# Kernel optimization log

Hardware: AMD Instinct MI355X
Metric: run time of the kernel (lower is better)

The kernel has to match this reference:

```python
import jax, jax.numpy as jnp
import numpy as np

D_MODEL = 1024
D_FF = 4096
BATCH = 4
SEQ = 2048
DECAY = 0.9
THRESH = 0.5


def setup_inputs() -> dict:
    key = jax.random.key(0)
    k1, k2, k3, k4 = jax.random.split(key, 4)
    spikes = jax.random.normal(k1, (BATCH, SEQ, D_MODEL), dtype=jnp.float32)
    # xavier-ish init scales matching gains 0.5/0.5/0.3 in the torch module
    s1 = 0.5 * np.sqrt(2.0 / (D_MODEL + D_FF))
    s2 = 0.5 * np.sqrt(2.0 / (D_MODEL + D_FF))
    sr = 0.3 * np.sqrt(2.0 / (D_MODEL + D_FF))
    W1 = jax.random.normal(k2, (D_FF, D_MODEL), dtype=jnp.float32) * s1
    W2 = jax.random.normal(k3, (D_MODEL, D_FF), dtype=jnp.float32) * s2
    Wr = jax.random.normal(k4, (D_FF, D_MODEL), dtype=jnp.float32) * sr
    return {"spikes": spikes, "W1": W1, "W2": W2, "Wr": Wr}


def reference(spikes, W1, W2, Wr):
    # spikes: [B, T, D]; W1, Wr: [F, D]; W2: [D, F]
    B, T, D = spikes.shape
    F = W1.shape[0]
    d = jnp.float32(DECAY)
    one_minus_d = jnp.float32(1.0 - DECAY)
    # Hoist time-independent projections out of the recurrence (same math as
    # the per-timestep nn.Linear calls in the torch loop).
    r_all = jax.nn.sigmoid(jnp.einsum('btd,fd->btf', spikes, Wr))  # [B,T,F]
    h_all = jnp.einsum('btd,fd->btf', spikes, W1)                   # [B,T,F]

    def step(carry, xs):
        act, rec = carry              # [B,F] each, init zeros (fresh buffers)
        r_t, h_t = xs                 # [B,F]
        rec = d * rec + one_minus_d * r_t                 # mixed receptance
        mixed = d * act + one_minus_d * h_t               # temporal state mix
        spike = (mixed > THRESH).astype(h_t.dtype)        # eval-mode spikes
        gated = spike * r_t
        # torch detaches current_activation each step
        return (jax.lax.stop_gradient(mixed), rec), gated

    init = (jnp.zeros((B, F), spikes.dtype), jnp.zeros((B, F), spikes.dtype))
    _, gated = jax.lax.scan(step,
                            init,
                            (jnp.swapaxes(r_all, 0, 1), jnp.swapaxes(h_all, 0, 1)))
    # gated: [T, B, F] -> output [B, T, D]
    out = jnp.einsum('tbf,df->btd', gated, W2)
    return out
```

## Files before the change

### kernel.cpp

```cpp
#include <hip/hip_runtime.h>
#include <math.h>

#define B_    4
#define T_    2048
#define D_    1024
#define F_    4096
#define R_    (B_*T_)
#define SEG_  64
#define L_    (T_/SEG_)
#define DECAYF 0.9f
#define OMDF   0.1f
#define FLAG_THRESH 0.45f

typedef __attribute__((ext_vector_type(4)))  int   i32x4;
typedef __attribute__((ext_vector_type(8)))  int   i32x8;
typedef __attribute__((ext_vector_type(16))) float f32x16;

__device__ __forceinline__ int pk_fp8x4(float x, float y, float z, float w) {
    int p = 0;
    p = __builtin_amdgcn_cvt_pk_fp8_f32(x, y, p, false);
    p = __builtin_amdgcn_cvt_pk_fp8_f32(z, w, p, true);
    return p;
}

__device__ __forceinline__ size_t pk_off(int row, int d) {
    return ((size_t)((row >> 5) * 16 + (d >> 6)) * 2048)
         + ((d >> 4) & 1) * 1024
         + ((row & 31) + ((d >> 5) & 1) * 32) * 16
         + (d & 15);
}

#define KA_W1_BLOCKS  4096
#define KA_SEG_BLOCKS 256
#define KA_FLAG_BLOCKS 32

__global__ __launch_bounds__(256)
void kA_prologue(const float* __restrict__ spikes,
                 const float* __restrict__ W1,
                 unsigned char* __restrict__ w_f8,
                 float* __restrict__ seg_sum,
                 unsigned int* __restrict__ flags) {
    const int bid = blockIdx.x;
    const int tid = threadIdx.x;
    if (bid < KA_W1_BLOCKS) {
        int i = bid * 256 + tid;
        float4 v = ((const float4*)W1)[i];
        int f  = i >> 8;
        int d0 = (i & 255) * 4;
        *(int*)(w_f8 + pk_off(f, d0)) = pk_fp8x4(8.f*v.x, 8.f*v.y, 8.f*v.z, 8.f*v.w);
    } else if (bid < KA_W1_BLOCKS + KA_SEG_BLOCKS) {
        int t = (bid - KA_W1_BLOCKS) * 256 + tid;
        int dg = t & (D_ / 4 - 1);
        int s = (t >> 8) & (SEG_ - 1);
        int b = t >> 14;
        const float4* sp4 = (const float4*)spikes;
        const int base = (b * T_ + s * L_) * (D_ / 4) + dg;
        float4 e = {0.f, 0.f, 0.f, 0.f};
#pragma unroll 8
        for (int k = 0; k < L_; ++k) {
            float4 x = sp4[base + k * (D_ / 4)];
            e.x = DECAYF * e.x + OMDF * x.x;
            e.y = DECAYF * e.y + OMDF * x.y;
            e.z = DECAYF * e.z + OMDF * x.z;
            e.w = DECAYF * e.w + OMDF * x.w;
        }
        ((float4*)seg_sum)[(b * SEG_ + s) * (D_ / 4) + dg] = e;
    } else {
        int i = (bid - KA_W1_BLOCKS - KA_SEG_BLOCKS) * 256 + tid;
        if (i < R_) flags[i] = 0u;
    }
}

__global__ __launch_bounds__(256)
void kB_seg_scan(const float* __restrict__ seg_sum,
                 float* __restrict__ start_state) {
    int g = blockIdx.x * 256 + threadIdx.x;
    int s = g & 63;
    int c = g >> 6;
    int d = c & (D_ - 1);
    int b = c >> 10;
    int idx = (b * SEG_ + s) * D_ + d;
    float v = seg_sum[idx];
    float wp = 0.0343368382f;
#pragma unroll
    for (int off = 1; off < SEG_; off <<= 1) {
        float u = __shfl_up(v, off, 64);
        if (s >= off) v += wp * u;
        wp *= wp;
    }
    float pv = __shfl_up(v, 1, 64);
    start_state[idx] = (s == 0) ? 0.f : pv;
}

__global__ __launch_bounds__(256)
void kC_ema_fp8(const float* __restrict__ spikes,
                const float* __restrict__ start_state,
                unsigned char* __restrict__ a_f8) {
    int t = blockIdx.x * 256 + threadIdx.x;
    int dg = t & (D_ / 4 - 1);
    int s = (t >> 8) & (SEG_ - 1);
    int b = t >> 14;
    const float4* sp4 = (const float4*)spikes;
    const int base = (b * T_ + s * L_) * (D_ / 4) + dg;
    const int d0 = dg * 4;
    unsigned char* dst = a_f8 + pk_off(b * T_ + s * L_, d0);
    float4 e = ((const float4*)start_state)[(b * SEG_ + s) * (D_ / 4) + dg];
#pragma unroll 8
    for (int k = 0; k < L_; ++k) {
        float4 x = sp4[base + k * (D_ / 4)];
        e.x = DECAYF * e.x + OMDF * x.x;
        e.y = DECAYF * e.y + OMDF * x.y;
        e.z = DECAYF * e.z + OMDF * x.z;
        e.w = DECAYF * e.w + OMDF * x.w;
        *(int*)(dst + k * 16) = pk_fp8x4(8.f*e.x, 8.f*e.y, 8.f*e.z, 8.f*e.w);
    }
}

__global__ __launch_bounds__(256)
void k2_mfma_flags(const unsigned char* __restrict__ Ap,
                   const unsigned char* __restrict__ Bp,
                   unsigned int* __restrict__ flags) {
    const int tid = threadIdx.x;
    const int w = tid >> 6;
    const int lane = tid & 63;
    const int orig = blockIdx.x;
    const int xcd  = orig & 7;
    const int id   = orig >> 3;
    const int mt   = (xcd >> 1) * 16 + (id >> 4);
    const int nt   = (xcd & 1) * 16 + (id & 15);
    const int m0 = mt * 128;
    const int n0 = nt * 128;
    const int wm = w >> 1, wn = w & 1;
    const int kg = lane >> 5;

    const unsigned char* pa0 = Ap + ((size_t)((m0 >> 5) + wm * 2 + 0) * 16) * 2048 + lane * 16;
    const unsigned char* pa1 = Ap + ((size_t)((m0 >> 5) + wm * 2 + 1) * 16) * 2048 + lane * 16;
    const unsigned char* pb0 = Bp + ((size_t)((n0 >> 5) + wn * 2 + 0) * 16) * 2048 + lane * 16;
    const unsigned char* pb1 = Bp + ((size_t)((n0 >> 5) + wn * 2 + 1) * 16) * 2048 + lane * 16;

    f32x16 acc[2][2] = {};

#define LDFRAG(p, C)                                                        \
    ({ i32x4 lo_ = *(const i32x4*)((p) + (size_t)(C) * 2048);               \
       i32x4 hi_ = *(const i32x4*)((p) + (size_t)(C) * 2048 + 1024);        \
       (i32x8){lo_.x, lo_.y, lo_.z, lo_.w, hi_.x, hi_.y, hi_.z, hi_.w}; })

#define MFMA4(AF0, AF1, BF0, BF1)                                           \
    {                                                                       \
        acc[0][0] = __builtin_amdgcn_mfma_scale_f32_32x32x64_f8f6f4(        \
            AF0, BF0, acc[0][0], 0, 0, 0, 124, 0, 124);                     \
        acc[0][1] = __builtin_amdgcn_mfma_scale_f32_32x32x64_f8f6f4(        \
            AF0, BF1, acc[0][1], 0, 0, 0, 124, 0, 124);                     \
        acc[1][0] = __builtin_amdgcn_mfma_scale_f32_32x32x64_f8f6f4(        \
            AF1, BF0, acc[1][0], 0, 0, 0, 124, 0, 124);                     \
        acc[1][1] = __builtin_amdgcn_mfma_scale_f32_32x32x64_f8f6f4(        \
            AF1, BF1, acc[1][1], 0, 0, 0, 124, 0, 124);                     \
    }

#pragma unroll
    for (int C = 0; C < 16; ++C) {
        __syncthreads();
        __builtin_amdgcn_sched_barrier(0);
        i32x8 A0 = LDFRAG(pa0, C), A1 = LDFRAG(pa1, C);
        i32x8 B0 = LDFRAG(pb0, C), B1 = LDFRAG(pb1, C);
        MFMA4(A0, A1, B0, B1);
    }
#undef LDFRAG
#undef MFMA4

#pragma unroll
    for (int i = 0; i < 2; ++i) {
#pragma unroll
        for (int reg = 0; reg < 16; ++reg) {
            float mx = fmaxf(acc[i][0][reg], acc[i][1][reg]);
            if (mx > FLAG_THRESH) {
                const int rr = (reg & 3) + 8 * (reg >> 2) + 4 * kg;
                atomicOr(&flags[m0 + wm * 64 + i * 32 + rr], 1u);
            }
        }
    }
}

__global__ __launch_bounds__(256)
void k4_output(const float* __restrict__ spikes,
               const float* __restrict__ start_state,
               const float* __restrict__ W1,
               const float* __restrict__ Wr,
               const float* __restrict__ W2,
               const unsigned int* __restrict__ flags,
               float* __restrict__ out) {
    const int row = blockIdx.x;
    const int tid = threadIdx.x;
    float4 o = {0.f, 0.f, 0.f, 0.f};

    if (flags[row] == 0u) {
        *(float4*)&out[(size_t)row * D_ + tid * 4] = o;
        return;
    }

    __shared__ float se[D_];
    __shared__ float sp[D_];
    __shared__ float red[256];
    __shared__ int nspk;
    __shared__ int spk_list[256];

    const int b = row / T_;
    const int t = row % T_;
    const int seg = t / L_;
    const int off = t % L_;
    const int segbase = (b * T_ + seg * L_) * D_;

    for (int i = tid; i < D_; i += 256) {
        float e = start_state[(b * SEG_ + seg) * D_ + i];
        for (int j = 0; j <= off; ++j)
            e = DECAYF * e + OMDF * spikes[segbase + j * D_ + i];
        se[i] = e;
        sp[i] = spikes[(size_t)row * D_ + i];
    }
    if (tid == 0) nspk = 0;
    __syncthreads();

    for (int f0 = 0; f0 < F_; f0 += 256) {
        int f = f0 + tid;
        float mix = 0.f;
        for (int k = 0; k < D_; ++k) mix += se[k] * W1[(size_t)f * D_ + k];
        if (mix > 0.5f) {
            int idx = atomicAdd(&nspk, 1);
            spk_list[idx] = f;
        }
        __syncthreads();
        int n = nspk;
        for (int i = 0; i < n; ++i) {
            int fs = spk_list[i];
            float part = 0.f;
#pragma unroll
            for (int k = 0; k < 4; ++k)
                part += sp[tid * 4 + k] * Wr[(size_t)fs * D_ + tid * 4 + k];
            red[tid] = part;
            __syncthreads();
            for (int sft = 128; sft > 0; sft >>= 1) {
                if (tid < sft) red[tid] += red[tid + sft];
                __syncthreads();
            }
            float r = 1.f / (1.f + expf(-red[0]));
            __syncthreads();
            o.x += r * W2[(size_t)(tid * 4 + 0) * F_ + fs];
            o.y += r * W2[(size_t)(tid * 4 + 1) * F_ + fs];
            o.z += r * W2[(size_t)(tid * 4 + 2) * F_ + fs];
            o.w += r * W2[(size_t)(tid * 4 + 3) * F_ + fs];
        }
        __syncthreads();
        if (tid == 0) nspk = 0;
        __syncthreads();
    }
    *(float4*)&out[(size_t)row * D_ + tid * 4] = o;
}

extern "C" void kernel_launch(void* const* d_in, const int* in_sizes, int n_in,
                              void* d_out, int out_size, void* d_ws, size_t ws_size,
                              hipStream_t stream) {
    const float* spikes = (const float*)d_in[0];
    const float* W1     = (const float*)d_in[1];
    const float* W2     = (const float*)d_in[2];
    const float* Wr     = (const float*)d_in[3];
    float* out = (float*)d_out;

    char* ws = (char*)d_ws;
    float* seg_sum      = (float*)ws;
    float* start_state  = seg_sum + (size_t)B_ * SEG_ * D_;
    unsigned int* flags = (unsigned int*)(start_state + (size_t)B_ * SEG_ * D_);
    unsigned char* a_f8 = (unsigned char*)(flags + R_);
    unsigned char* w_f8 = a_f8 + (size_t)R_ * D_;

    kA_prologue<<<KA_W1_BLOCKS + KA_SEG_BLOCKS + KA_FLAG_BLOCKS, 256, 0, stream>>>(
        spikes, W1, w_f8, seg_sum, flags);
    kB_seg_scan<<<(B_ * D_ * 64) / 256, 256, 0, stream>>>(seg_sum, start_state);
    kC_ema_fp8<<<(B_ * SEG_ * D_ / 4) / 256, 256, 0, stream>>>(spikes, start_state, a_f8);

    k2_mfma_flags<<<(R_ / 128) * (F_ / 128), 256, 0, stream>>>(a_f8, w_f8, flags);

    k4_output<<<R_, 256, 0, stream>>>(spikes, start_state, W1, Wr, W2, flags, out);
}
```

Measured before the change: 202.9 us.

## Stage flag-GEMM tiles through double-buffered LDS via global_load_lds

The flag-computing FP8 MFMA kernel now copies A and B tiles into a double-buffered shared-memory staging area using direct global-to-LDS loads. Each wave fetches one quarter of the tile, and the next K chunk is prefetched while the current one is consumed. Before, every wave read its own fragments straight from global memory, so tiles shared between waves were fetched twice. The block-to-tile swizzle is also changed so that each XCD gets a contiguous range of tiles. In exchange the kernel uses 32KB of LDS per block and adds barrier traffic, and there is no wait on the async LDS load's vmcnt before the barrier, which may be a correctness risk.

```diff
diff --git a/kernel.cpp b/kernel.cpp
--- a/kernel.cpp
+++ b/kernel.cpp
@@ -11,6 +11,7 @@
 #define DECAYF 0.9f
 #define OMDF   0.1f
 #define FLAG_THRESH 0.45f
+
 
 typedef __attribute__((ext_vector_type(4)))  int   i32x4;
 typedef __attribute__((ext_vector_type(8)))  int   i32x8;
@@ -124,25 +125,48 @@
     const int w = tid >> 6;
     const int lane = tid & 63;
     const int orig = blockIdx.x;
-    const int xcd  = orig & 7;
-    const int id   = orig >> 3;
-    const int mt   = (xcd >> 1) * 16 + (id >> 4);
-    const int nt   = (xcd & 1) * 16 + (id & 15);
-    const int m0 = mt * 128;
-    const int n0 = nt * 128;
+    const int swz  = (orig & 7) * 256 + (orig >> 3);
+    const int m0 = (swz >> 5) * 128;
+    const int n0 = (swz & 31) * 128;
     const int wm = w >> 1, wn = w & 1;
     const int kg = lane >> 5;
 
-    const unsigned char* pa0 = Ap + ((size_t)((m0 >> 5) + wm * 2 + 0) * 16) * 2048 + lane * 16;
-    const unsigned char* pa1 = Ap + ((size_t)((m0 >> 5) + wm * 2 + 1) * 16) * 2048 + lane * 16;
-    const unsigned char* pb0 = Bp + ((size_t)((n0 >> 5) + wn * 2 + 0) * 16) * 2048 + lane * 16;
-    const unsigned char* pb1 = Bp + ((size_t)((n0 >> 5) + wn * 2 + 1) * 16) * 2048 + lane * 16;
+    __shared__ unsigned char lbuf[2][16384];
+
+    const unsigned char* g0;
+    const unsigned char* g1;
+    if (w < 2) {
+        g0 = Ap + ((size_t)((m0 >> 5) + 2 * w    ) * 16) * 2048 + lane * 16;
+        g1 = Ap + ((size_t)((m0 >> 5) + 2 * w + 1) * 16) * 2048 + lane * 16;
+    } else {
+        g0 = Bp + ((size_t)((n0 >> 5) + 2 * (w - 2)    ) * 16) * 2048 + lane * 16;
+        g1 = Bp + ((size_t)((n0 >> 5) + 2 * (w - 2) + 1) * 16) * 2048 + lane * 16;
+    }
+    const int lt0 = (2 * w) * 2048;
+    const int lt1 = (2 * w + 1) * 2048;
+
+#define GLDS(gp, loff)                                                      \
+    __builtin_amdgcn_global_load_lds(                                       \
+        (const __attribute__((address_space(1))) void*)(gp),                \
+        (__attribute__((address_space(3))) void*)(&lbuf[0][0] + (loff)),    \
+        16, 0, 0)
+
+#define STAGE(C, buf)                                                       \
+    GLDS(g0 + (size_t)(C) * 2048,        (buf) * 16384 + lt0);              \
+    GLDS(g0 + (size_t)(C) * 2048 + 1024, (buf) * 16384 + lt0 + 1024);       \
+    GLDS(g1 + (size_t)(C) * 2048,        (buf) * 16384 + lt1);              \
+    GLDS(g1 + (size_t)(C) * 2048 + 1024, (buf) * 16384 + lt1 + 1024);
 
     f32x16 acc[2][2] = {};
 
-#define LDFRAG(p, C)                                                        \
-    ({ i32x4 lo_ = *(const i32x4*)((p) + (size_t)(C) * 2048);               \
-       i32x4 hi_ = *(const i32x4*)((p) + (size_t)(C) * 2048 + 1024);        \
+    const int aoff0 = (wm * 2    ) * 2048 + lane * 16;
+    const int aoff1 = (wm * 2 + 1) * 2048 + lane * 16;
+    const int boff0 = (4 + wn * 2    ) * 2048 + lane * 16;
+    const int boff1 = (4 + wn * 2 + 1) * 2048 + lane * 16;
+
+#define LDSF(off, buf)                                                      \
+    ({ i32x4 lo_ = *(const i32x4*)(&lbuf[0][0] + (buf) * 16384 + (off));    \
+       i32x4 hi_ = *(const i32x4*)(&lbuf[0][0] + (buf) * 16384 + (off) + 1024); \
        (i32x8){lo_.x, lo_.y, lo_.z, lo_.w, hi_.x, hi_.y, hi_.z, hi_.w}; })
 
 #define MFMA4(AF0, AF1, BF0, BF1)                                           \
@@ -157,15 +181,21 @@
             AF1, BF1, acc[1][1], 0, 0, 0, 124, 0, 124);                     \
     }
 
+    STAGE(0, 0)
+    __syncthreads();
+
 #pragma unroll
     for (int C = 0; C < 16; ++C) {
-        __syncthreads();
-        __builtin_amdgcn_sched_barrier(0);
-        i32x8 A0 = LDFRAG(pa0, C), A1 = LDFRAG(pa1, C);
-        i32x8 B0 = LDFRAG(pb0, C), B1 = LDFRAG(pb1, C);
+        const int buf = C & 1;
+        if (C < 15) { STAGE(C + 1, buf ^ 1) }
+        i32x8 A0 = LDSF(aoff0, buf), A1 = LDSF(aoff1, buf);
+        i32x8 B0 = LDSF(boff0, buf), B1 = LDSF(boff1, buf);
         MFMA4(A0, A1, B0, B1);
-    }
-#undef LDFRAG
+        if (C < 15) __syncthreads();
+    }
+#undef GLDS
+#undef STAGE
+#undef LDSF
 #undef MFMA4
 
 #pragma unroll
```

After: 205.3 us. About the same (+1.2%).
